# Kernel tuning notes

Hardware: AMD Instinct MI355X
Metric: run time of the kernel (lower is better)

## Reference

```python
import jax, jax.numpy as jnp
import numpy as np

ALPHA = 0.6
K = 4


def gsdnef_conv(x, edge_index, W, b, alpha, K):
    """SpGSDNEFConv: linear transform then K-step graph-signal-denoising diffusion
    h_{k+1} = (x + alpha * A_hat h_k) / (1 + alpha), A_hat = D^-1/2 (A+I) D^-1/2."""
    n = x.shape[0]
    x = x @ W + b  # [N, C_out]
    loop = jnp.arange(n, dtype=edge_index.dtype)
    src = jnp.concatenate([edge_index[0], loop])
    dst = jnp.concatenate([edge_index[1], loop])
    ones = jnp.ones(src.shape, dtype=x.dtype)
    deg = jax.ops.segment_sum(ones, dst, num_segments=n)
    dinv = jax.lax.rsqrt(jnp.maximum(deg, 1e-12))
    norm = dinv[src] * dinv[dst]  # [E+N]
    inv = 1.0 / (1.0 + alpha)
    h = x
    for _ in range(K):
        agg = jax.ops.segment_sum(h[src] * norm[:, None], dst, num_segments=n)
        h = (x + alpha * agg) * inv
    return h


def setup_inputs() -> dict:
    key = jax.random.key(0)
    ks = jax.random.split(key, 16)
    N, E, C_in, H, C_out = 50000, 800000, 256, 128, 64
    x = jax.random.normal(ks[0], (N, C_in), dtype=jnp.float32)
    edge_index = jax.random.randint(ks[1], (2, E), 0, N, dtype=jnp.int64)

    def lin(k, fan_in, fan_out):
        k1, k2 = jax.random.split(k)
        bound = 1.0 / np.sqrt(fan_in)
        W = jax.random.uniform(k1, (fan_in, fan_out), jnp.float32, -bound, bound)
        b = jax.random.uniform(k2, (fan_out,), jnp.float32, -bound, bound)
        return W, b

    Wc1, bc1 = lin(ks[2], C_in, H)
    Wl1, bl1 = lin(ks[3], C_in, H)
    Wc2, bc2 = lin(ks[4], H, H)
    Wl2, bl2 = lin(ks[5], H, H)
    Wc3, bc3 = lin(ks[6], H, C_out)
    Wl3, bl3 = lin(ks[7], H, C_out)
    return dict(x=x, edge_index=edge_index,
                Wc1=Wc1, bc1=bc1, Wl1=Wl1, bl1=bl1,
                Wc2=Wc2, bc2=bc2, Wl2=Wl2, bl2=bl2,
                Wc3=Wc3, bc3=bc3, Wl3=Wl3, bl3=bl3)


def reference(x, edge_index, Wc1, bc1, Wl1, bl1, Wc2, bc2, Wl2, bl2, Wc3, bc3, Wl3, bl3):
    h = jax.nn.elu(gsdnef_conv(x, edge_index, Wc1, bc1, ALPHA, K) + (x @ Wl1 + bl1))
    h = jax.nn.elu(gsdnef_conv(h, edge_index, Wc2, bc2, ALPHA, K) + (h @ Wl2 + bl2))
    h = gsdnef_conv(h, edge_index, Wc3, bc3, ALPHA, K) + (h @ Wl3 + bl3)
    return h
```

## Files before the change

kernel.cpp:

```cpp
#include <hip/hip_runtime.h>
#include <hip/hip_fp16.h>
#include <math.h>

#define ALPHA_C 0.6f

typedef _Float16 f16;
typedef f16 f16x8 __attribute__((ext_vector_type(8)));
typedef float f32x4 __attribute__((ext_vector_type(4)));

__global__ void f32_to_f16_kernel(const float* __restrict__ in, f16* __restrict__ out, int n8) {
    int i = blockIdx.x * blockDim.x + threadIdx.x;
    if (i >= n8) return;
    float4 a = ((const float4*)in)[2 * i];
    float4 b = ((const float4*)in)[2 * i + 1];
    f16x8 o;
    o[0] = (f16)a.x; o[1] = (f16)a.y; o[2] = (f16)a.z; o[3] = (f16)a.w;
    o[4] = (f16)b.x; o[5] = (f16)b.y; o[6] = (f16)b.z; o[7] = (f16)b.w;
    ((f16x8*)out)[i] = o;
}

__global__ void detect_idx_kernel(const void* __restrict__ ei, int* __restrict__ flag,
                                  int E, int N) {
    int i = blockIdx.x * blockDim.x + threadIdx.x;
    if (i >= E) return;
    long long v = ((const long long*)ei)[i];
    if (v < 0 || v >= (long long)N) *flag = 1;
}

__global__ void convert_count_kernel(const void* __restrict__ ei, const int* __restrict__ flag,
                                     int* __restrict__ out, int* __restrict__ cnt,
                                     int E, int n2e) {
    int i = blockIdx.x * blockDim.x + threadIdx.x;
    if (i >= n2e) return;
    int v;
    if (*flag == 0)
        v = (int)((const long long*)ei)[i];
    else
        v = ((const int*)ei)[i];
    out[i] = v;
    if (i >= E) atomicAdd(&cnt[v], 1);
}

__global__ void block_reduce_kernel(const int* __restrict__ cnt, int* __restrict__ bsum,
                                    float* __restrict__ dinv, int n) {
    __shared__ int s[256];
    int tid = threadIdx.x;
    int i = blockIdx.x * 256 + tid;
    int v = (i < n) ? cnt[i] : 0;
    if (i < n) dinv[i] = rsqrtf((float)v + 1.0f);
    s[tid] = v;
    __syncthreads();
    for (int o = 128; o > 0; o >>= 1) {
        if (tid < o) s[tid] += s[tid + o];
        __syncthreads();
    }
    if (tid == 0) bsum[blockIdx.x] = s[0];
}

__global__ void scan_top_kernel(int* __restrict__ bsum, int nb) {
    __shared__ int s[1024];
    int tid = threadIdx.x;
    int v = (tid < nb) ? bsum[tid] : 0;
    s[tid] = v;
    __syncthreads();
    for (int o = 1; o < 1024; o <<= 1) {
        int t = (tid >= o) ? s[tid - o] : 0;
        __syncthreads();
        s[tid] += t;
        __syncthreads();
    }
    if (tid < nb) bsum[tid] = s[tid] - v;
}

__global__ void scan_fill_kernel(const int* __restrict__ cnt, const int* __restrict__ bsum,
                                 int* __restrict__ row_off, int* __restrict__ gcur, int n) {
    __shared__ int s[256];
    int tid = threadIdx.x;
    int i = blockIdx.x * 256 + tid;
    int v = (i < n) ? cnt[i] : 0;
    s[tid] = v;
    __syncthreads();
    for (int o = 1; o < 256; o <<= 1) {
        int t = (tid >= o) ? s[tid - o] : 0;
        __syncthreads();
        s[tid] += t;
        __syncthreads();
    }
    int base = bsum[blockIdx.x];
    if (i < n) {
        int ro = base + s[tid] - v;
        row_off[i] = ro;
        if ((i & 255) == 0) gcur[i >> 8] = ro;
    }
    if (i == n - 1) row_off[n] = base + s[tid];
}

__global__ __launch_bounds__(256) void bucket_scatter_kernel(
    const int* __restrict__ src, const int* __restrict__ dst,
    int* __restrict__ gcur, unsigned int* __restrict__ ebuf, int E, int NB) {
    __shared__ int hist[256];
    __shared__ int loff[256];
    __shared__ int lbase[256];
    __shared__ int lcur[256];
    __shared__ unsigned int lbuf[2048];
    int tid = threadIdx.x;
    int e0 = blockIdx.x * 2048;
    int ecnt = E - e0; if (ecnt > 2048) ecnt = 2048;

    hist[tid] = 0; lcur[tid] = 0;
    __syncthreads();
    for (int i = tid; i < ecnt; i += 256)
        atomicAdd(&hist[(unsigned)dst[e0 + i] >> 8], 1);
    __syncthreads();
    loff[tid] = hist[tid];
    __syncthreads();
    for (int o = 1; o < 256; o <<= 1) {
        int v = (tid >= o) ? loff[tid - o] : 0;
        __syncthreads();
        loff[tid] += v;
        __syncthreads();
    }
    {
        int h = hist[tid];
        lbase[tid] = (tid < NB && h) ? atomicAdd(&gcur[tid], h) : 0;
    }
    __syncthreads();
    for (int i = tid; i < ecnt; i += 256) {
        int d = dst[e0 + i], s = src[e0 + i];
        int b = (unsigned)d >> 8;
        int p = atomicAdd(&lcur[b], 1);
        lbuf[loff[b] - hist[b] + p] = (unsigned)s | ((unsigned)d << 16);
    }
    __syncthreads();
    for (int i = tid; i < ecnt; i += 256) {
        unsigned int pr = lbuf[i];
        int b = (pr >> 16) >> 8;
        int rel = i - (loff[b] - hist[b]);
        ebuf[lbase[b] + rel] = pr;
    }
}

__global__ __launch_bounds__(256) void csr_finalize_kernel(
    const unsigned int* __restrict__ ebuf, const int* __restrict__ row_off,
    const float* __restrict__ dinv, unsigned int* __restrict__ csre, int N) {
    __shared__ int lcur[256];
    __shared__ unsigned int lbuf[6144];
    int b = blockIdx.x;
    int n0 = b * 256;
    int n1 = n0 + 256; if (n1 > N) n1 = N;
    int base = row_off[n0];
    int cnt = row_off[n1] - base;
    int tid = threadIdx.x;
    lcur[tid] = 0;
    __syncthreads();
    bool fits = (cnt <= 6144);
    for (int i = tid; i < cnt; i += 256) {
        unsigned int pr = ebuf[base + i];
        int s = pr & 0xFFFF;
        int d = pr >> 16;
        float w = dinv[s] * dinv[d];
        unsigned int entry = (unsigned)s |
                             ((unsigned)__half_as_ushort(__float2half(w)) << 16);
        int rel = row_off[d] - base;
        int p = atomicAdd(&lcur[d - n0], 1);
        if (fits) lbuf[rel + p] = entry;
        else      csre[base + rel + p] = entry;
    }
    __syncthreads();
    if (fits)
        for (int i = tid; i < cnt; i += 256) csre[base + i] = lbuf[i];
}

__global__ void prep_all_w_kernel(
    const float* __restrict__ Wc1, const float* __restrict__ Wl1,
    const float* __restrict__ Wc2, const float* __restrict__ Wl2,
    const float* __restrict__ Wc3, const float* __restrict__ Wl3,
    f16* __restrict__ w1c, f16* __restrict__ w1l,
    f16* __restrict__ w2c, f16* __restrict__ w2l,
    f16* __restrict__ w3c, f16* __restrict__ w3l) {
    int i = blockIdx.x * blockDim.x + threadIdx.x;
    const float* W; f16* O; int K, Nn, base;
    if      (i <  32768) { W = Wc1; O = w1c; K = 256; Nn = 128; base = i; }
    else if (i <  65536) { W = Wl1; O = w1l; K = 256; Nn = 128; base = i - 32768; }
    else if (i <  81920) { W = Wc2; O = w2c; K = 128; Nn = 128; base = i - 65536; }
    else if (i <  98304) { W = Wl2; O = w2l; K = 128; Nn = 128; base = i - 81920; }
    else if (i < 106496) { W = Wc3; O = w3c; K = 128; Nn = 64;  base = i - 98304; }
    else if (i < 114688) { W = Wl3; O = w3l; K = 128; Nn = 64;  base = i - 106496; }
    else return;
    int k = base / Nn, n = base - k * Nn;
    O[(size_t)n * K + k] = (f16)W[base];
}

template <int K, int NH, int AMODE, int SPLIT>
__global__ __launch_bounds__(256) void gemm2_kernel(
    const void* __restrict__ A0v, const void* __restrict__ A1v,
    const f16* __restrict__ WtA, const f16* __restrict__ WtB,
    const float* __restrict__ biasA, const float* __restrict__ biasB,
    f16* __restrict__ CA, f16* __restrict__ CB, int M) {
    constexpr int NT = 2 * NH / 16;
    constexpr int NTS = NT / SPLIT;
    constexpr int KS = K / 32;
    __shared__ f16 Wlds[NTS * 1024];

    int tid = threadIdx.x;
    int wv = tid >> 6, lane = tid & 63;
    int lr = lane & 15, lhi = lane >> 4;
    int m0 = blockIdx.x * 64;
    int tg0 = blockIdx.y * NTS;

    f32x4 acc[NTS];
#pragma unroll
    for (int t = 0; t < NTS; ++t) acc[t] = (f32x4){0.f, 0.f, 0.f, 0.f};

    int arow = m0 + wv * 16 + lr;
    int arow_c = arow < M ? arow : M - 1;
    size_t aoff = (size_t)arow_c * K + lhi * 8;

    f16x8 a[KS];
#pragma unroll
    for (int j = 0; j < KS; ++j) {
        size_t idx = aoff + j * 32;
        if constexpr (AMODE == 0) {
            a[j] = *(const f16x8*)((const f16*)A0v + idx);
        } else {
            f16x8 u0 = *(const f16x8*)((const f16*)A0v + idx);
            f16x8 u1 = *(const f16x8*)((const f16*)A1v + idx);
            f16x8 v;
#pragma unroll
            for (int jj = 0; jj < 8; ++jj) {
                float tt = (float)u0[jj] + (float)u1[jj];
                v[jj] = (f16)(tt > 0.f ? tt : expm1f(tt));
            }
            a[j] = v;
        }
    }

#pragma unroll
    for (int k0 = 0; k0 < K; k0 += 64) {
        for (int c = tid; c < NTS * 128; c += 256) {
            int tl = c >> 7;
            int rem = c & 127;
            int ks = rem >> 6, kh = (rem >> 4) & 3, r = rem & 15;
            int tg = tg0 + tl;
            int nloc = (tg < NT / 2) ? tg : tg - NT / 2;
            const f16* srcp = ((tg < NT / 2) ? WtA : WtB)
                              + (size_t)(nloc * 16 + r) * K + k0 + ks * 32 + kh * 8;
            *(f16x8*)&Wlds[(size_t)c * 8] = *(const f16x8*)srcp;
        }
        __syncthreads();

#pragma unroll
        for (int s2 = 0; s2 < 2; ++s2) {
#pragma unroll
            for (int t = 0; t < NTS; ++t) {
                f16x8 b = *(const f16x8*)&Wlds[(size_t)(t * 128 + s2 * 64 + lane) * 8];
                acc[t] = __builtin_amdgcn_mfma_f32_16x16x32_f16(a[k0 / 32 + s2], b, acc[t], 0, 0, 0);
            }
        }
        __syncthreads();
    }

    int rbase = m0 + wv * 16 + lhi * 4;
#pragma unroll
    for (int t = 0; t < NTS; ++t) {
        int tg = tg0 + t;
        bool isA = (tg < NT / 2);
        int colg = (isA ? tg : tg - NT / 2) * 16 + lr;
        f16* outp = isA ? CA : CB;
        float bv = (isA ? biasA : biasB)[colg];
#pragma unroll
        for (int r = 0; r < 4; ++r) {
            int row = rbase + r;
            if (row < M) outp[(size_t)row * NH + colg] = (f16)(acc[t][r] + bv);
        }
    }
}

template <int C, bool FINAL>
__global__ __launch_bounds__(256) void diffuse16_kernel(
    const __half* __restrict__ h, const __half* __restrict__ xc,
    const float* __restrict__ dinv, const int* __restrict__ row_off,
    const unsigned int* __restrict__ csre, __half* __restrict__ hout,
    const f16* __restrict__ lin, float* __restrict__ fout, int N) {
    const float inv = 1.0f / (1.0f + ALPHA_C);
    int gid = blockIdx.x * blockDim.x + threadIdx.x;
    int node = gid >> 6;
    if (node >= N) return;
    int lane = threadIdx.x & 63;
    float di = dinv[node];
    float di2 = di * di;
    int e0 = row_off[node], e1 = row_off[node + 1];

    if constexpr (C == 128) {
        int l = lane & 15, grp = lane >> 4;
        float acc[8];
#pragma unroll
        for (int i = 0; i < 8; ++i) acc[i] = 0.f;
        size_t coff = (size_t)l * 8;

        if (grp == 0) {
            float4 rv = *(const float4*)(h + ((size_t)node << 7) + coff);
            const __half2* p = (const __half2*)&rv;
#pragma unroll
            for (int k = 0; k < 4; ++k) {
                float2 f = __half22float2(p[k]);
                acc[2 * k] += di2 * f.x;
                acc[2 * k + 1] += di2 * f.y;
            }
        }
        int e = e0 + grp;
        for (; e + 12 < e1; e += 16) {
            unsigned int ev0 = csre[e], ev1 = csre[e + 4], ev2 = csre[e + 8], ev3 = csre[e + 12];
            float4 r0 = *(const float4*)(h + ((size_t)(ev0 & 0xFFFF) << 7) + coff);
            float4 r1 = *(const float4*)(h + ((size_t)(ev1 & 0xFFFF) << 7) + coff);
            float4 r2 = *(const float4*)(h + ((size_t)(ev2 & 0xFFFF) << 7) + coff);
            float4 r3 = *(const float4*)(h + ((size_t)(ev3 & 0xFFFF) << 7) + coff);
            float w0 = __half2float(__ushort_as_half((unsigned short)(ev0 >> 16)));
            float w1 = __half2float(__ushort_as_half((unsigned short)(ev1 >> 16)));
            float w2 = __half2float(__ushort_as_half((unsigned short)(ev2 >> 16)));
            float w3 = __half2float(__ushort_as_half((unsigned short)(ev3 >> 16)));
            const __half2* p0 = (const __half2*)&r0;
            const __half2* p1 = (const __half2*)&r1;
            const __half2* p2 = (const __half2*)&r2;
            const __half2* p3 = (const __half2*)&r3;
#pragma unroll
            for (int k = 0; k < 4; ++k) {
                float2 f0 = __half22float2(p0[k]);
                float2 f1 = __half22float2(p1[k]);
                float2 f2 = __half22float2(p2[k]);
                float2 f3 = __half22float2(p3[k]);
                acc[2 * k]     += w0 * f0.x + w1 * f1.x + w2 * f2.x + w3 * f3.x;
                acc[2 * k + 1] += w0 * f0.y + w1 * f1.y + w2 * f2.y + w3 * f3.y;
            }
        }
        for (; e < e1; e += 4) {
            unsigned int ev0 = csre[e];
            float4 r0 = *(const float4*)(h + ((size_t)(ev0 & 0xFFFF) << 7) + coff);
            float w0 = __half2float(__ushort_as_half((unsigned short)(ev0 >> 16)));
            const __half2* p0 = (const __half2*)&r0;
#pragma unroll
            for (int k = 0; k < 4; ++k) {
                float2 f0 = __half22float2(p0[k]);
                acc[2 * k]     += w0 * f0.x;
                acc[2 * k + 1] += w0 * f0.y;
            }
        }
#pragma unroll
        for (int i = 0; i < 8; ++i) {
            acc[i] += __shfl_xor(acc[i], 16);
            acc[i] += __shfl_xor(acc[i], 32);
        }
        if (grp == 0) {
            float4 xv = *(const float4*)(xc + ((size_t)node << 7) + coff);
            const __half2* xp = (const __half2*)&xv;
            __half ov[8];
#pragma unroll
            for (int k = 0; k < 4; ++k) {
                float2 xf = __half22float2(xp[k]);
                ov[2 * k]     = __float2half((xf.x + ALPHA_C * acc[2 * k]) * inv);
                ov[2 * k + 1] = __float2half((xf.y + ALPHA_C * acc[2 * k + 1]) * inv);
            }
            *(float4*)(hout + ((size_t)node << 7) + coff) = *(float4*)ov;
        }
    } else {
        int l = lane & 7, grp = lane >> 3;
        float acc[8];
#pragma unroll
        for (int i = 0; i < 8; ++i) acc[i] = 0.f;
        size_t coff = (size_t)l * 8;

        if (grp == 0) {
            float4 rv = *(const float4*)(h + ((size_t)node << 6) + coff);
            const __half2* p = (const __half2*)&rv;
#pragma unroll
            for (int k = 0; k < 4; ++k) {
                float2 f = __half22float2(p[k]);
                acc[2 * k] += di2 * f.x;
                acc[2 * k + 1] += di2 * f.y;
            }
        }
        int e = e0 + grp;
        for (; e + 8 < e1; e += 16) {
            unsigned int ev0 = csre[e], ev1 = csre[e + 8];
            float4 r0 = *(const float4*)(h + ((size_t)(ev0 & 0xFFFF) << 6) + coff);
            float4 r1 = *(const float4*)(h + ((size_t)(ev1 & 0xFFFF) << 6) + coff);
            float w0 = __half2float(__ushort_as_half((unsigned short)(ev0 >> 16)));
            float w1 = __half2float(__ushort_as_half((unsigned short)(ev1 >> 16)));
            const __half2* p0 = (const __half2*)&r0;
            const __half2* p1 = (const __half2*)&r1;
#pragma unroll
            for (int k = 0; k < 4; ++k) {
                float2 f0 = __half22float2(p0[k]);
                float2 f1 = __half22float2(p1[k]);
                acc[2 * k]     += w0 * f0.x + w1 * f1.x;
                acc[2 * k + 1] += w0 * f0.y + w1 * f1.y;
            }
        }
        if (e < e1) {
            unsigned int ev0 = csre[e];
            float4 r0 = *(const float4*)(h + ((size_t)(ev0 & 0xFFFF) << 6) + coff);
            float w0 = __half2float(__ushort_as_half((unsigned short)(ev0 >> 16)));
            const __half2* p0 = (const __half2*)&r0;
#pragma unroll
            for (int k = 0; k < 4; ++k) {
                float2 f0 = __half22float2(p0[k]);
                acc[2 * k]     += w0 * f0.x;
                acc[2 * k + 1] += w0 * f0.y;
            }
        }
#pragma unroll
        for (int i = 0; i < 8; ++i) {
            acc[i] += __shfl_xor(acc[i], 8);
            acc[i] += __shfl_xor(acc[i], 16);
            acc[i] += __shfl_xor(acc[i], 32);
        }
        if (grp == 0) {
            float4 xv = *(const float4*)(xc + ((size_t)node << 6) + coff);
            const __half2* xp = (const __half2*)&xv;
            float r[8];
#pragma unroll
            for (int k = 0; k < 4; ++k) {
                float2 xf = __half22float2(xp[k]);
                r[2 * k]     = (xf.x + ALPHA_C * acc[2 * k]) * inv;
                r[2 * k + 1] = (xf.y + ALPHA_C * acc[2 * k + 1]) * inv;
            }
            if constexpr (FINAL) {
                f16x8 lv = *(const f16x8*)(lin + ((size_t)node << 6) + coff);
                float4 o0, o1;
                o0.x = r[0] + (float)lv[0]; o0.y = r[1] + (float)lv[1];
                o0.z = r[2] + (float)lv[2]; o0.w = r[3] + (float)lv[3];
                o1.x = r[4] + (float)lv[4]; o1.y = r[5] + (float)lv[5];
                o1.z = r[6] + (float)lv[6]; o1.w = r[7] + (float)lv[7];
                float* op = fout + ((size_t)node << 6) + coff;
                *(float4*)op = o0;
                *(float4*)(op + 4) = o1;
            } else {
                __half ov[8];
#pragma unroll
                for (int k = 0; k < 8; ++k) ov[k] = __float2half(r[k]);
                *(float4*)(hout + ((size_t)node << 6) + coff) = *(float4*)ov;
            }
        }
    }
}

extern "C" void kernel_launch(void* const* d_in, const int* in_sizes, int n_in,
                              void* d_out, int out_size, void* d_ws, size_t ws_size,
                              hipStream_t stream) {
    const float* x   = (const float*)d_in[0];
    const void*  ei  = d_in[1];
    const float* Wc1 = (const float*)d_in[2];  const float* bc1 = (const float*)d_in[3];
    const float* Wl1 = (const float*)d_in[4];  const float* bl1 = (const float*)d_in[5];
    const float* Wc2 = (const float*)d_in[6];  const float* bc2 = (const float*)d_in[7];
    const float* Wl2 = (const float*)d_in[8];  const float* bl2 = (const float*)d_in[9];
    const float* Wc3 = (const float*)d_in[10]; const float* bc3 = (const float*)d_in[11];
    const float* Wl3 = (const float*)d_in[12]; const float* bl3 = (const float*)d_in[13];
    float* out = (float*)d_out;

    const int N = in_sizes[0] / 256;
    const int E = in_sizes[1] / 2;
    const int NB = (N + 255) >> 8;

    size_t off = 0;
    auto alloc = [&](size_t bytes) {
        void* p = (char*)d_ws + off;
        off += (bytes + 255) & ~(size_t)255;
        return p;
    };
    f16* x16 = (f16*)alloc((size_t)N * 256 * 2);
    f16* B0 = (f16*)alloc((size_t)N * 128 * 2);
    f16* B1 = (f16*)alloc((size_t)N * 128 * 2);
    f16* B2 = (f16*)alloc((size_t)N * 128 * 2);
    f16* B3 = (f16*)alloc((size_t)N * 128 * 2);
    f16* B4 = (f16*)alloc((size_t)N * 128 * 2);
    f16* wt1c = (f16*)alloc((size_t)256 * 128 * 2);
    f16* wt1l = (f16*)alloc((size_t)256 * 128 * 2);
    f16* wt2c = (f16*)alloc((size_t)128 * 128 * 2);
    f16* wt2l = (f16*)alloc((size_t)128 * 128 * 2);
    f16* wt3c = (f16*)alloc((size_t)128 * 64 * 2);
    f16* wt3l = (f16*)alloc((size_t)128 * 64 * 2);
    float* dinv   = (float*)alloc((size_t)N * 4);
    int*   zreg   = (int*)  alloc((size_t)(N + 64) * 4);
    int*   flag   = zreg;
    int*   cnt    = zreg + 64;
    int*   rowoff = (int*)  alloc((size_t)(N + 1) * 4);
    int*   bsum   = (int*)  alloc(1024 * 4);
    int*   gcur   = (int*)  alloc(1024 * 4);
    unsigned int* csre = (unsigned int*)alloc((size_t)E * 4);
    unsigned int* ebuf = (unsigned int*)alloc((size_t)E * 4);
    int*   idx32  = (int*)  alloc((size_t)2 * E * 4);
    int* src32 = idx32;
    int* dst32 = idx32 + E;

    const int TB = 256;
    int ge  = (E + TB - 1) / TB;
    int g2e = (2 * E + TB - 1) / TB;
    int nb  = (N + 255) / 256;

    hipMemsetAsync(zreg, 0, (size_t)(N + 64) * 4, stream);

    int gx8 = (N * 256 / 8 + TB - 1) / TB;
    f32_to_f16_kernel<<<gx8, TB, 0, stream>>>(x, x16, N * 256 / 8);

    detect_idx_kernel<<<ge, TB, 0, stream>>>(ei, flag, E, N);
    convert_count_kernel<<<g2e, TB, 0, stream>>>(ei, flag, idx32, cnt, E, 2 * E);

    block_reduce_kernel<<<nb, 256, 0, stream>>>(cnt, bsum, dinv, N);
    scan_top_kernel<<<1, 1024, 0, stream>>>(bsum, nb);
    scan_fill_kernel<<<nb, 256, 0, stream>>>(cnt, bsum, rowoff, gcur, N);
    int gbk = (E + 2047) / 2048;
    bucket_scatter_kernel<<<gbk, 256, 0, stream>>>(src32, dst32, gcur, ebuf, E, NB);
    csr_finalize_kernel<<<NB, 256, 0, stream>>>(ebuf, rowoff, dinv, csre, N);

    prep_all_w_kernel<<<(114688 + TB - 1) / TB, TB, 0, stream>>>(
        Wc1, Wl1, Wc2, Wl2, Wc3, Wl3, wt1c, wt1l, wt2c, wt2l, wt3c, wt3l);

    dim3 gm((N + 63) / 64, 2);
    int gd = (N * 64 + TB - 1) / TB;

    gemm2_kernel<256, 128, 0, 2><<<gm, TB, 0, stream>>>(x16, nullptr, wt1c, wt1l, bc1, bl1, B0, B1, N);
    diffuse16_kernel<128, false><<<gd, TB, 0, stream>>>((__half*)B0, (__half*)B0, dinv, rowoff, csre, (__half*)B2, nullptr, nullptr, N);
    diffuse16_kernel<128, false><<<gd, TB, 0, stream>>>((__half*)B2, (__half*)B0, dinv, rowoff, csre, (__half*)B3, nullptr, nullptr, N);
    diffuse16_kernel<128, false><<<gd, TB, 0, stream>>>((__half*)B3, (__half*)B0, dinv, rowoff, csre, (__half*)B2, nullptr, nullptr, N);
    diffuse16_kernel<128, false><<<gd, TB, 0, stream>>>((__half*)B2, (__half*)B0, dinv, rowoff, csre, (__half*)B3, nullptr, nullptr, N);

    gemm2_kernel<128, 128, 2, 2><<<gm, TB, 0, stream>>>(B3, B1, wt2c, wt2l, bc2, bl2, B0, B4, N);
    diffuse16_kernel<128, false><<<gd, TB, 0, stream>>>((__half*)B0, (__half*)B0, dinv, rowoff, csre, (__half*)B1, nullptr, nullptr, N);
    diffuse16_kernel<128, false><<<gd, TB, 0, stream>>>((__half*)B1, (__half*)B0, dinv, rowoff, csre, (__half*)B2, nullptr, nullptr, N);
    diffuse16_kernel<128, false><<<gd, TB, 0, stream>>>((__half*)B2, (__half*)B0, dinv, rowoff, csre, (__half*)B1, nullptr, nullptr, N);
    diffuse16_kernel<128, false><<<gd, TB, 0, stream>>>((__half*)B1, (__half*)B0, dinv, rowoff, csre, (__half*)B2, nullptr, nullptr, N);

    gemm2_kernel<128, 64, 2, 2><<<gm, TB, 0, stream>>>(B2, B4, wt3c, wt3l, bc3, bl3, B0, B1, N);
    diffuse16_kernel<64, false><<<gd, TB, 0, stream>>>((__half*)B0, (__half*)B0, dinv, rowoff, csre, (__half*)B2, nullptr, nullptr, N);
    diffuse16_kernel<64, false><<<gd, TB, 0, stream>>>((__half*)B2, (__half*)B0, dinv, rowoff, csre, (__half*)B3, nullptr, nullptr, N);
    diffuse16_kernel<64, false><<<gd, TB, 0, stream>>>((__half*)B3, (__half*)B0, dinv, rowoff, csre, (__half*)B2, nullptr, nullptr, N);
    diffuse16_kernel<64, true ><<<gd, TB, 0, stream>>>((__half*)B2, (__half*)B0, dinv, rowoff, csre, nullptr, B1, out, N);
}
```

Measured before the change: 546.2 us.

## Replace per-node degree counting and scans with bucket-level histogram CSR build

The per-node global atomic degree count and the three-kernel hierarchical scan are replaced by a grid-stride kernel that keeps a shared-memory histogram over 256-node buckets, plus a single-block bucket scan. Per-node row offsets and dinv are now derived after the bucket scatter by a new kernel that counts nodes per bucket in shared memory and scans locally. This removes the large N-sized memset, the global atomics on 50k counters, and two launches, at the cost of an extra pass over the edge buffer. The scan assumes NB is at most 256.

```diff
diff --git a/kernel.cpp b/kernel.cpp
--- a/kernel.cpp
+++ b/kernel.cpp
@@ -27,57 +27,29 @@
     if (v < 0 || v >= (long long)N) *flag = 1;
 }
 
-__global__ void convert_count_kernel(const void* __restrict__ ei, const int* __restrict__ flag,
-                                     int* __restrict__ out, int* __restrict__ cnt,
-                                     int E, int n2e) {
-    int i = blockIdx.x * blockDim.x + threadIdx.x;
-    if (i >= n2e) return;
-    int v;
-    if (*flag == 0)
-        v = (int)((const long long*)ei)[i];
-    else
-        v = ((const int*)ei)[i];
-    out[i] = v;
-    if (i >= E) atomicAdd(&cnt[v], 1);
-}
-
-__global__ void block_reduce_kernel(const int* __restrict__ cnt, int* __restrict__ bsum,
-                                    float* __restrict__ dinv, int n) {
+__global__ __launch_bounds__(256) void convert_hist_kernel(
+    const void* __restrict__ ei, const int* __restrict__ flag,
+    int* __restrict__ out, int* __restrict__ bcnt, int E, int n2e) {
+    __shared__ int hist[256];
+    int tid = threadIdx.x;
+    hist[tid] = 0;
+    __syncthreads();
+    bool is64 = (*flag == 0);
+    for (int i = blockIdx.x * 256 + tid; i < n2e; i += gridDim.x * 256) {
+        int v = is64 ? (int)((const long long*)ei)[i] : ((const int*)ei)[i];
+        out[i] = v;
+        if (i >= E) atomicAdd(&hist[(unsigned)v >> 8], 1);
+    }
+    __syncthreads();
+    int h = hist[tid];
+    if (h) atomicAdd(&bcnt[tid], h);
+}
+
+__global__ void bucket_scan_kernel(const int* __restrict__ bcnt, int* __restrict__ boff,
+                                   int* __restrict__ gcur, int NB) {
     __shared__ int s[256];
     int tid = threadIdx.x;
-    int i = blockIdx.x * 256 + tid;
-    int v = (i < n) ? cnt[i] : 0;
-    if (i < n) dinv[i] = rsqrtf((float)v + 1.0f);
-    s[tid] = v;
-    __syncthreads();
-    for (int o = 128; o > 0; o >>= 1) {
-        if (tid < o) s[tid] += s[tid + o];
-        __syncthreads();
-    }
-    if (tid == 0) bsum[blockIdx.x] = s[0];
-}
-
-__global__ void scan_top_kernel(int* __restrict__ bsum, int nb) {
-    __shared__ int s[1024];
-    int tid = threadIdx.x;
-    int v = (tid < nb) ? bsum[tid] : 0;
-    s[tid] = v;
-    __syncthreads();
-    for (int o = 1; o < 1024; o <<= 1) {
-        int t = (tid >= o) ? s[tid - o] : 0;
-        __syncthreads();
-        s[tid] += t;
-        __syncthreads();
-    }
-    if (tid < nb) bsum[tid] = s[tid] - v;
-}
-
-__global__ void scan_fill_kernel(const int* __restrict__ cnt, const int* __restrict__ bsum,
-                                 int* __restrict__ row_off, int* __restrict__ gcur, int n) {
-    __shared__ int s[256];
-    int tid = threadIdx.x;
-    int i = blockIdx.x * 256 + tid;
-    int v = (i < n) ? cnt[i] : 0;
+    int v = (tid < NB) ? bcnt[tid] : 0;
     s[tid] = v;
     __syncthreads();
     for (int o = 1; o < 256; o <<= 1) {
@@ -86,13 +58,9 @@
         s[tid] += t;
         __syncthreads();
     }
-    int base = bsum[blockIdx.x];
-    if (i < n) {
-        int ro = base + s[tid] - v;
-        row_off[i] = ro;
-        if ((i & 255) == 0) gcur[i >> 8] = ro;
-    }
-    if (i == n - 1) row_off[n] = base + s[tid];
+    int ex = s[tid] - v;
+    if (tid < NB) { boff[tid] = ex; gcur[tid] = ex; }
+    if (tid == NB - 1) boff[NB] = ex + v;
 }
 
 __global__ __launch_bounds__(256) void bucket_scatter_kernel(
@@ -137,6 +105,38 @@
         int b = (pr >> 16) >> 8;
         int rel = i - (loff[b] - hist[b]);
         ebuf[lbase[b] + rel] = pr;
+    }
+}
+
+__global__ __launch_bounds__(256) void finalize_a_kernel(
+    const unsigned int* __restrict__ ebuf, const int* __restrict__ boff,
+    int* __restrict__ row_off, float* __restrict__ dinv, int N) {
+    __shared__ int ncnt[256];
+    __shared__ int ps[256];
+    int b = blockIdx.x;
+    int n0 = b << 8;
+    int base = boff[b];
+    int cnt = boff[b + 1] - base;
+    int tid = threadIdx.x;
+    ncnt[tid] = 0;
+    __syncthreads();
+    for (int i = tid; i < cnt; i += 256)
+        atomicAdd(&ncnt[(int)(ebuf[base + i] >> 16) - n0], 1);
+    __syncthreads();
+    int v = ncnt[tid];
+    ps[tid] = v;
+    __syncthreads();
+    for (int o = 1; o < 256; o <<= 1) {
+        int t = (tid >= o) ? ps[tid - o] : 0;
+        __syncthreads();
+        ps[tid] += t;
+        __syncthreads();
+    }
+    int node = n0 + tid;
+    if (node < N) {
+        row_off[node] = base + ps[tid] - v;
+        dinv[node] = rsqrtf((float)v + 1.0f);
+        if (node == N - 1) row_off[N] = base + ps[tid];
     }
 }
 
@@ -480,12 +480,12 @@
     f16* wt3c = (f16*)alloc((size_t)128 * 64 * 2);
     f16* wt3l = (f16*)alloc((size_t)128 * 64 * 2);
     float* dinv   = (float*)alloc((size_t)N * 4);
-    int*   zreg   = (int*)  alloc((size_t)(N + 64) * 4);
+    int*   zreg   = (int*)  alloc((size_t)(64 + 256) * 4);
     int*   flag   = zreg;
-    int*   cnt    = zreg + 64;
+    int*   bcnt   = zreg + 64;
     int*   rowoff = (int*)  alloc((size_t)(N + 1) * 4);
-    int*   bsum   = (int*)  alloc(1024 * 4);
-    int*   gcur   = (int*)  alloc(1024 * 4);
+    int*   boff   = (int*)  alloc(257 * 4);
+    int*   gcur   = (int*)  alloc(256 * 4);
     unsigned int* csre = (unsigned int*)alloc((size_t)E * 4);
     unsigned int* ebuf = (unsigned int*)alloc((size_t)E * 4);
     int*   idx32  = (int*)  alloc((size_t)2 * E * 4);
@@ -494,22 +494,19 @@
 
     const int TB = 256;
     int ge  = (E + TB - 1) / TB;
-    int g2e = (2 * E + TB - 1) / TB;
-    int nb  = (N + 255) / 256;
-
-    hipMemsetAsync(zreg, 0, (size_t)(N + 64) * 4, stream);
+
+    hipMemsetAsync(zreg, 0, (size_t)(64 + 256) * 4, stream);
 
     int gx8 = (N * 256 / 8 + TB - 1) / TB;
     f32_to_f16_kernel<<<gx8, TB, 0, stream>>>(x, x16, N * 256 / 8);
 
     detect_idx_kernel<<<ge, TB, 0, stream>>>(ei, flag, E, N);
-    convert_count_kernel<<<g2e, TB, 0, stream>>>(ei, flag, idx32, cnt, E, 2 * E);
-
-    block_reduce_kernel<<<nb, 256, 0, stream>>>(cnt, bsum, dinv, N);
-    scan_top_kernel<<<1, 1024, 0, stream>>>(bsum, nb);
-    scan_fill_kernel<<<nb, 256, 0, stream>>>(cnt, bsum, rowoff, gcur, N);
+    convert_hist_kernel<<<480, TB, 0, stream>>>(ei, flag, idx32, bcnt, E, 2 * E);
+
+    bucket_scan_kernel<<<1, 256, 0, stream>>>(bcnt, boff, gcur, NB);
     int gbk = (E + 2047) / 2048;
     bucket_scatter_kernel<<<gbk, 256, 0, stream>>>(src32, dst32, gcur, ebuf, E, NB);
+    finalize_a_kernel<<<NB, 256, 0, stream>>>(ebuf, boff, rowoff, dinv, N);
     csr_finalize_kernel<<<NB, 256, 0, stream>>>(ebuf, rowoff, dinv, csre, N);
 
     prep_all_w_kernel<<<(114688 + TB - 1) / TB, TB, 0, stream>>>(
```

After: 521.3 us (median of 2 runs). 1.05x faster.
